# Performance work log

Hardware: AMD Instinct MI355X
Metric: run time of the kernel (lower is better)

Reference implementation:

```python
import jax, jax.numpy as jnp
import numpy as np

N, D, DFF, E, K = 2048, 1024, 4096, 8, 2  # tokens, d_model, d_ff, num_expert, top_k


def setup_inputs() -> dict:
    key = jax.random.key(0)
    ks = jax.random.split(key, 5)
    s = 0.02  # init scale
    return {
        "moe_inp": jax.random.normal(ks[0], (N, D), jnp.float32),
        "Wg": jax.random.normal(ks[1], (D, E), jnp.float32) * s,   # gate linear
        "bg": jnp.zeros((E,), jnp.float32),
        "W1": jax.random.normal(ks[2], (E, D, DFF), jnp.float32) * s,  # htoh4 per expert
        "b1": jnp.zeros((E, DFF), jnp.float32),
        "W2": jax.random.normal(ks[3], (E, DFF, D), jnp.float32) * s,  # h4toh per expert
        "b2": jnp.zeros((E, D), jnp.float32),
    }


def reference(moe_inp, Wg, bg, W1, b1, W2, b2):
    # --- NaiveGate: top-k experts per token, softmax over selected logits ---
    logits = moe_inp @ Wg + bg                      # [N, E]
    top_val, top_idx = jax.lax.top_k(logits, K)     # [N, K]
    score = jax.nn.softmax(top_val, axis=-1)        # [N, K]

    # Dense combine weights c[n, e] = sum_j score[n, j] * 1{top_idx[n, j] == e}.
    # This is the mathematically exact equivalent of scatter -> grouped expert
    # GEMM -> gather -> score-weighted combine in fmoe.
    comb = jnp.einsum(
        "nke,nk->ne", jax.nn.one_hot(top_idx, E, dtype=moe_inp.dtype), score
    )                                               # [N, E]

    # --- per-expert FFN: relu(x W1 + b1) W2 + b2, masked-combined by comb ---
    h = jax.nn.relu(jnp.einsum("nd,edh->enh", moe_inp, W1) + b1[:, None, :])  # [E, N, DFF]
    out = jnp.einsum("enh,ehd,ne->nd", h, W2, comb) + comb @ b2               # [N, D]
    return out
```

## Files before the change

### kernel.cpp

```cpp
#include <hip/hip_runtime.h>
#include <hip/hip_bf16.h>
#include <cstdint>
#include <cstddef>

#define NTOKS  2048
#define DMODEL 1024
#define DFFN   4096
#define NEXP   8
#define TSLOTS 40

typedef __attribute__((ext_vector_type(8))) short short8;
typedef __attribute__((ext_vector_type(4))) float f32x4;
typedef __attribute__((ext_vector_type(4))) unsigned short u16x4;
typedef __attribute__((ext_vector_type(8))) unsigned short u16x8;

static constexpr size_t alignup(size_t x) { return (x + 255) & ~(size_t)255; }
static constexpr size_t OFF_XB   = 0;
static constexpr size_t OFF_CNT  = alignup(OFF_XB + (size_t)(NTOKS + 1) * DMODEL * 2);
static constexpr size_t OFF_OFFS = OFF_CNT + 256;
static constexpr size_t OFF_TOKE = OFF_OFFS + 256;
static constexpr size_t OFF_TOKT = OFF_TOKE + (size_t)NTOKS * 2 * 4;
static constexpr size_t OFF_TOKS = OFF_TOKT + (size_t)NTOKS * 2 * 4;
static constexpr size_t OFF_TI   = alignup(OFF_TOKS + (size_t)NTOKS * 2 * 4);
static constexpr size_t OFF_CAP  = alignup(OFF_TI + 512);
static constexpr size_t OFF_H    = alignup(OFF_CAP + (size_t)NEXP * NTOKS * 4);
static constexpr size_t OFF_Y    = alignup(OFF_H + (size_t)(NTOKS * 2 + 128) * DFFN * 2);
static constexpr size_t OFF_WB   = alignup(OFF_Y + (size_t)2 * NTOKS * 2 * DMODEL * 4);

__device__ inline unsigned short f2bf(float f) {
  __hip_bfloat16 h = __float2bfloat16(f);
  return __builtin_bit_cast(unsigned short, h);
}

__device__ inline void gload16(const void* g, void* l) {
  __builtin_amdgcn_global_load_lds((const __attribute__((address_space(1))) unsigned int*)g,
                                   (__attribute__((address_space(3))) unsigned int*)l, 16, 0, 0);
}

__global__ __launch_bounds__(256) void k_convert(const float* __restrict__ x,
                                                 unsigned short* __restrict__ xb,
                                                 int* __restrict__ cnt) {
  if (blockIdx.x == 0 && threadIdx.x < NEXP) cnt[threadIdx.x] = 0;
  size_t base = ((size_t)blockIdx.x * 256 + threadIdx.x) * 8;
  const size_t total = (size_t)(NTOKS + 1) * DMODEL;
  if (base >= total) return;
  u16x8 o;
  if (base < (size_t)NTOKS * DMODEL) {
    f32x4 a = *(const f32x4*)(x + base);
    f32x4 b = *(const f32x4*)(x + base + 4);
#pragma unroll
    for (int j = 0; j < 4; ++j) { o[j] = f2bf(a[j]); o[4 + j] = f2bf(b[j]); }
  } else {
#pragma unroll
    for (int j = 0; j < 8; ++j) o[j] = 0;
  }
  *(u16x8*)(xb + base) = o;
}

template <int R, int C>
__global__ __launch_bounds__(256) void k_transconv(const float* __restrict__ W,
                                                   unsigned short* __restrict__ WT) {
  __shared__ unsigned short T[64][66];
  const int e = blockIdx.z;
  const int c0 = blockIdx.x * 64, r0 = blockIdx.y * 64;
  const float* Wp = W + (size_t)e * R * C;
  unsigned short* Tp = WT + (size_t)e * R * C;
  const int tid = threadIdx.x;
  const int rr = tid >> 4, cc = (tid & 15) << 2;
#pragma unroll
  for (int i = 0; i < 4; ++i) {
    int r = rr + (i << 4);
    f32x4 v = *(const f32x4*)(Wp + (size_t)(r0 + r) * C + c0 + cc);
    T[r][cc]     = f2bf(v[0]);
    T[r][cc + 1] = f2bf(v[1]);
    T[r][cc + 2] = f2bf(v[2]);
    T[r][cc + 3] = f2bf(v[3]);
  }
  __syncthreads();
  const int c = tid >> 2, kc = (tid & 3) << 4;
  u16x8 o0, o1;
#pragma unroll
  for (int i = 0; i < 8; ++i) { o0[i] = T[kc + i][c]; o1[i] = T[kc + 8 + i][c]; }
  unsigned short* dst = Tp + (size_t)(c0 + c) * R + r0 + kc;
  *(u16x8*)(dst) = o0;
  *(u16x8*)(dst + 8) = o1;
}

__global__ __launch_bounds__(256) void k_gate(const float* __restrict__ x,
                                              const float* __restrict__ Wg,
                                              const float* __restrict__ bg,
                                              int* __restrict__ cnt,
                                              int* __restrict__ tok_e,
                                              int* __restrict__ tok_t,
                                              float* __restrict__ tok_s,
                                              int* __restrict__ cap) {
  const int w = threadIdx.x >> 6, lane = threadIdx.x & 63;
  const int n = blockIdx.x * 4 + w;
  float acc[8];
#pragma unroll
  for (int e = 0; e < 8; ++e) acc[e] = 0.f;
  const float* xr = x + (size_t)n * DMODEL;
#pragma unroll 4
  for (int it = 0; it < DMODEL / 64; ++it) {
    int d = it * 64 + lane;
    float xv = xr[d];
    f32x4 w0 = *(const f32x4*)(Wg + d * 8);
    f32x4 w1 = *(const f32x4*)(Wg + d * 8 + 4);
#pragma unroll
    for (int j = 0; j < 4; ++j) { acc[j] += xv * w0[j]; acc[4 + j] += xv * w1[j]; }
  }
#pragma unroll
  for (int e = 0; e < 8; ++e)
#pragma unroll
    for (int off = 32; off; off >>= 1) acc[e] += __shfl_xor(acc[e], off, 64);
  if (lane == 0) {
    float l[8];
#pragma unroll
    for (int e = 0; e < 8; ++e) l[e] = acc[e] + bg[e];
    int i0 = 0; float v0 = l[0];
#pragma unroll
    for (int e = 1; e < 8; ++e) if (l[e] > v0) { v0 = l[e]; i0 = e; }
    int i1 = (i0 == 0) ? 1 : 0; float v1 = l[i1];
#pragma unroll
    for (int e = 0; e < 8; ++e) if (e != i0 && l[e] > v1) { v1 = l[e]; i1 = e; }
    float t = expf(v1 - v0);
    float inv = 1.f / (1.f + t);
    float s0 = inv, s1 = t * inv;
    int t0 = atomicAdd(&cnt[i0], 1);
    int t1 = atomicAdd(&cnt[i1], 1);
    cap[i0 * NTOKS + t0] = n;
    cap[i1 * NTOKS + t1] = n;
    tok_e[2 * n] = i0; tok_e[2 * n + 1] = i1;
    tok_t[2 * n] = t0; tok_t[2 * n + 1] = t1;
    tok_s[2 * n] = s0; tok_s[2 * n + 1] = s1;
  }
}

__global__ void k_scan(const int* __restrict__ cnt, int* __restrict__ offs,
                       int2* __restrict__ tinfo) {
  if (threadIdx.x == 0) {
    int s = 0;
#pragma unroll
    for (int e = 0; e < NEXP; ++e) { offs[e] = s; s += cnt[e]; }
    int ns = 0;
    for (int e = 0; e < NEXP; ++e)
      for (int t = 0; t * 128 < cnt[e]; ++t) { tinfo[ns] = make_int2(e, t * 128); ++ns; }
    for (; ns < TSLOTS; ++ns) tinfo[ns] = make_int2(-1, 0);
  }
}

template <int KTOT, int NTOT, int BN, bool FIRST, int KSPLIT>
__global__ __launch_bounds__(256) void k_gemm(const unsigned short* __restrict__ Asrc,
                                              const unsigned short* __restrict__ Bsrc,
                                              const float* __restrict__ bias,
                                              const int* __restrict__ cnt,
                                              const int* __restrict__ offs,
                                              const int2* __restrict__ tinfo,
                                              const int* __restrict__ cap,
                                              unsigned short* __restrict__ hout,
                                              float* __restrict__ yout) {
  const int2 ti = tinfo[blockIdx.y];
  if (ti.x < 0) return;
  const int e = ti.x, t0 = ti.y;
  const int c = cnt[e];
  const int base = offs[e] + t0;
  const int n0 = blockIdx.x * BN;
  constexpr int KCH = KTOT / KSPLIT;
  constexpr int NT = KCH / 32;
  const int kb = blockIdx.z * KCH;

  const int tid = threadIdx.x, w = tid >> 6, lane = tid & 63;
  const int l15 = lane & 15, lq = lane >> 4;
  constexpr int MR = 4;
  constexpr int NR = BN / 32;
  constexpr int BR = BN / 64;
  const int wr = w >> 1, wc = w & 1;

  __shared__ unsigned short As[2][128 * 32];
  __shared__ unsigned short Bs[2][BN * 32];

  const int rl = tid >> 2;
  const int sw = (((tid & 3) ^ (rl & 3) ^ ((rl >> 2) & 3)) << 3);
  const unsigned short* aptr[2];
#pragma unroll
  for (int r = 0; r < 2; ++r) {
    int row = r * 64 + rl;
    size_t gr;
    if constexpr (FIRST) gr = (size_t)((t0 + row < c) ? cap[e * NTOKS + t0 + row] : NTOKS);
    else                 gr = (size_t)(base + row);
    aptr[r] = Asrc + gr * (size_t)KTOT + kb + sw;
  }
  const unsigned short* Be = Bsrc + (size_t)e * ((size_t)KTOT * NTOT);
  const unsigned short* bptr[BR];
#pragma unroll
  for (int r = 0; r < BR; ++r)
    bptr[r] = Be + (size_t)(n0 + r * 64 + rl) * KTOT + kb + sw;

  auto stageA = [&](int k0, int b) {
#pragma unroll
    for (int r = 0; r < 2; ++r)
      gload16(aptr[r] + k0, &As[b][(r * 64 + w * 16) << 5]);
  };
  auto stageB = [&](int k0, int b) {
#pragma unroll
    for (int r = 0; r < BR; ++r)
      gload16(bptr[r] + k0, &Bs[b][(r * 64 + w * 16) << 5]);
  };

  f32x4 acc[MR][NR] = {};

  stageA(0, 0);
  stageB(0, 0);
  __syncthreads();

  int buf = 0;
  for (int t = 0; t < NT; ++t) {
    const int nxt = buf ^ 1;
    if (t + 1 < NT) { stageA((t + 1) * 32, nxt); stageB((t + 1) * 32, nxt); }

    short8 a[MR], b[NR];
    const int sw0 = ((lq ^ (l15 & 3) ^ ((l15 >> 2) & 3)) << 3);
#pragma unroll
    for (int m = 0; m < MR; ++m)
      a[m] = *(const short8*)&As[buf][((wr * 64 + m * 16 + l15) << 5) + sw0];
#pragma unroll
    for (int nn = 0; nn < NR; ++nn)
      b[nn] = *(const short8*)&Bs[buf][((wc * (BN / 2) + nn * 16 + l15) << 5) + sw0];
#pragma unroll
    for (int m = 0; m < MR; ++m)
#pragma unroll
      for (int nn = 0; nn < NR; ++nn)
        acc[m][nn] = __builtin_amdgcn_mfma_f32_16x16x32_bf16(a[m], b[nn], acc[m][nn], 0, 0, 0);

    __syncthreads();
    buf = nxt;
  }

  if constexpr (FIRST) {
    const float* be = bias + (size_t)e * NTOT;
#pragma unroll
    for (int m = 0; m < MR; ++m) {
#pragma unroll
      for (int q2 = 0; q2 < 4; ++q2) {
        int row = wr * 64 + m * 16 + lq * 4 + q2;
        if (t0 + row < c) {
          unsigned short* hr = hout + (size_t)(base + row) * NTOT;
#pragma unroll
          for (int nn = 0; nn < NR; ++nn) {
            int col = n0 + wc * (BN / 2) + nn * 16 + l15;
            float v = acc[m][nn][q2] + be[col];
            v = v > 0.f ? v : 0.f;
            hr[col] = f2bf(v);
          }
        }
      }
    }
  } else {
    float* yz = yout + (size_t)blockIdx.z * NTOKS * 2 * DMODEL;
#pragma unroll
    for (int m = 0; m < MR; ++m) {
#pragma unroll
      for (int q2 = 0; q2 < 4; ++q2) {
        int row = wr * 64 + m * 16 + lq * 4 + q2;
        if (t0 + row < c) {
          float* yr = yz + (size_t)(base + row) * NTOT;
#pragma unroll
          for (int nn = 0; nn < NR; ++nn) {
            int col = n0 + wc * (BN / 2) + nn * 16 + l15;
            yr[col] = acc[m][nn][q2];
          }
        }
      }
    }
  }
}

__global__ __launch_bounds__(256) void k_combine(const float* __restrict__ y,
                                                 const float* __restrict__ b2,
                                                 const int* __restrict__ tok_e,
                                                 const int* __restrict__ tok_t,
                                                 const float* __restrict__ tok_s,
                                                 const int* __restrict__ offs,
                                                 float* __restrict__ out) {
  const int n = blockIdx.x, t = threadIdx.x;
  const float* y1 = y + (size_t)NTOKS * 2 * DMODEL;
  const int e0 = tok_e[2 * n], e1 = tok_e[2 * n + 1];
  const int s0i = offs[e0] + tok_t[2 * n];
  const int s1i = offs[e1] + tok_t[2 * n + 1];
  const float sc0 = tok_s[2 * n], sc1 = tok_s[2 * n + 1];
  f32x4 v0 = *(const f32x4*)(y + (size_t)s0i * DMODEL + t * 4);
  f32x4 u0 = *(const f32x4*)(y1 + (size_t)s0i * DMODEL + t * 4);
  f32x4 v1 = *(const f32x4*)(y + (size_t)s1i * DMODEL + t * 4);
  f32x4 u1 = *(const f32x4*)(y1 + (size_t)s1i * DMODEL + t * 4);
  f32x4 c0 = *(const f32x4*)(b2 + (size_t)e0 * DMODEL + t * 4);
  f32x4 c1 = *(const f32x4*)(b2 + (size_t)e1 * DMODEL + t * 4);
  f32x4 r = sc0 * ((v0 + u0) + c0) + sc1 * ((v1 + u1) + c1);
  *(f32x4*)(out + (size_t)n * DMODEL + t * 4) = r;
}

extern "C" void kernel_launch(void* const* d_in, const int* in_sizes, int n_in,
                              void* d_out, int out_size, void* d_ws, size_t ws_size,
                              hipStream_t stream) {
  const float* x  = (const float*)d_in[0];
  const float* Wg = (const float*)d_in[1];
  const float* bg = (const float*)d_in[2];
  const float* W1 = (const float*)d_in[3];
  const float* b1 = (const float*)d_in[4];
  const float* W2 = (const float*)d_in[5];
  const float* b2 = (const float*)d_in[6];
  float* out = (float*)d_out;

  char* ws = (char*)d_ws;
  unsigned short* xb = (unsigned short*)(ws + OFF_XB);
  int*   cnt   = (int*)(ws + OFF_CNT);
  int*   offs  = (int*)(ws + OFF_OFFS);
  int*   tok_e = (int*)(ws + OFF_TOKE);
  int*   tok_t = (int*)(ws + OFF_TOKT);
  float* tok_s = (float*)(ws + OFF_TOKS);
  int2*  tinfo = (int2*)(ws + OFF_TI);
  int*   cap   = (int*)(ws + OFF_CAP);
  unsigned short* h  = (unsigned short*)(ws + OFF_H);
  float* y = (float*)(ws + OFF_Y);
  unsigned short* wb = (unsigned short*)(ws + OFF_WB);

  const int convBlocks = (int)(((size_t)(NTOKS + 1) * DMODEL / 8 + 255) / 256);
  k_convert<<<convBlocks, 256, 0, stream>>>(x, xb, cnt);
  k_gate<<<NTOKS / 4, 256, 0, stream>>>(x, Wg, bg, cnt, tok_e, tok_t, tok_s, cap);
  k_scan<<<1, 64, 0, stream>>>(cnt, offs, tinfo);

  k_transconv<DMODEL, DFFN><<<dim3(DFFN / 64, DMODEL / 64, NEXP), 256, 0, stream>>>(W1, wb);
  k_gemm<DMODEL, DFFN, 128, true, 1><<<dim3(DFFN / 128, TSLOTS, 1), 256, 0, stream>>>(
      xb, wb, b1, cnt, offs, tinfo, cap, h, nullptr);

  k_transconv<DFFN, DMODEL><<<dim3(DMODEL / 64, DFFN / 64, NEXP), 256, 0, stream>>>(W2, wb);
  k_gemm<DFFN, DMODEL, 64, false, 2><<<dim3(DMODEL / 64, TSLOTS, 2), 256, 0, stream>>>(
      h, wb, nullptr, cnt, offs, tinfo, cap, nullptr, y);

  k_combine<<<NTOKS, 256, 0, stream>>>(y, b2, tok_e, tok_t, tok_s, offs, out);
}
```

Before: 282.6 us.

## Merge prep kernels and overlap W2 conversion with first expert GEMM

Folds the W1 transpose/convert, input bf16 conversion and gating into one launch, and runs the first grouped GEMM and the W2 transpose/convert as one launch using separate weight buffers. This removes several launch boundaries and lets independent conversion work fill idle CUs during the GEMM. The counter reset moves to a memset. Y now aliases the W1 buffer, which is safe because W1 is dead by the time y is written. Mixed-role blocks share one grid, so LDS and register allocation follow the largest body, which may reduce occupancy.

```diff
diff --git a/kernel.cpp b/kernel.cpp
--- a/kernel.cpp
+++ b/kernel.cpp
@@ -7,7 +7,7 @@
 #define DMODEL 1024
 #define DFFN   4096
 #define NEXP   8
-#define TSLOTS 40
+#define TS128  40
 
 typedef __attribute__((ext_vector_type(8))) short short8;
 typedef __attribute__((ext_vector_type(4))) float f32x4;
@@ -21,11 +21,12 @@
 static constexpr size_t OFF_TOKE = OFF_OFFS + 256;
 static constexpr size_t OFF_TOKT = OFF_TOKE + (size_t)NTOKS * 2 * 4;
 static constexpr size_t OFF_TOKS = OFF_TOKT + (size_t)NTOKS * 2 * 4;
-static constexpr size_t OFF_TI   = alignup(OFF_TOKS + (size_t)NTOKS * 2 * 4);
-static constexpr size_t OFF_CAP  = alignup(OFF_TI + 512);
+static constexpr size_t OFF_TI2  = alignup(OFF_TOKS + (size_t)NTOKS * 2 * 4);
+static constexpr size_t OFF_CAP  = alignup(OFF_TI2 + TS128 * 8);
 static constexpr size_t OFF_H    = alignup(OFF_CAP + (size_t)NEXP * NTOKS * 4);
-static constexpr size_t OFF_Y    = alignup(OFF_H + (size_t)(NTOKS * 2 + 128) * DFFN * 2);
-static constexpr size_t OFF_WB   = alignup(OFF_Y + (size_t)2 * NTOKS * 2 * DMODEL * 4);
+static constexpr size_t OFF_WBA  = alignup(OFF_H + (size_t)(NTOKS * 2 + 128) * DFFN * 2);
+static constexpr size_t OFF_WBB  = alignup(OFF_WBA + (size_t)NEXP * DMODEL * DFFN * 2);
+static constexpr size_t OFF_Y    = OFF_WBA;
 
 __device__ inline unsigned short f2bf(float f) {
   __hip_bfloat16 h = __float2bfloat16(f);
@@ -37,11 +38,10 @@
                                    (__attribute__((address_space(3))) unsigned int*)l, 16, 0, 0);
 }
 
-__global__ __launch_bounds__(256) void k_convert(const float* __restrict__ x,
-                                                 unsigned short* __restrict__ xb,
-                                                 int* __restrict__ cnt) {
-  if (blockIdx.x == 0 && threadIdx.x < NEXP) cnt[threadIdx.x] = 0;
-  size_t base = ((size_t)blockIdx.x * 256 + threadIdx.x) * 8;
+
+__device__ __forceinline__ void conv_body(const float* __restrict__ x,
+                                          unsigned short* __restrict__ xb, int vb) {
+  size_t base = ((size_t)vb * 256 + threadIdx.x) * 8;
   const size_t total = (size_t)(NTOKS + 1) * DMODEL;
   if (base >= total) return;
   u16x8 o;
@@ -58,11 +58,12 @@
 }
 
 template <int R, int C>
-__global__ __launch_bounds__(256) void k_transconv(const float* __restrict__ W,
-                                                   unsigned short* __restrict__ WT) {
-  __shared__ unsigned short T[64][66];
-  const int e = blockIdx.z;
-  const int c0 = blockIdx.x * 64, r0 = blockIdx.y * 64;
+__device__ __forceinline__ void tc_body(const float* __restrict__ W,
+                                        unsigned short* __restrict__ WT,
+                                        int bx, int by, int bz,
+                                        unsigned short (*T)[66]) {
+  const int e = bz;
+  const int c0 = bx * 64, r0 = by * 64;
   const float* Wp = W + (size_t)e * R * C;
   unsigned short* Tp = WT + (size_t)e * R * C;
   const int tid = threadIdx.x;
@@ -86,16 +87,16 @@
   *(u16x8*)(dst + 8) = o1;
 }
 
-__global__ __launch_bounds__(256) void k_gate(const float* __restrict__ x,
-                                              const float* __restrict__ Wg,
-                                              const float* __restrict__ bg,
-                                              int* __restrict__ cnt,
-                                              int* __restrict__ tok_e,
-                                              int* __restrict__ tok_t,
-                                              float* __restrict__ tok_s,
-                                              int* __restrict__ cap) {
+__device__ __forceinline__ void gate_body(const float* __restrict__ x,
+                                          const float* __restrict__ Wg,
+                                          const float* __restrict__ bg,
+                                          int* __restrict__ cnt,
+                                          int* __restrict__ tok_e,
+                                          int* __restrict__ tok_t,
+                                          float* __restrict__ tok_s,
+                                          int* __restrict__ cap, int vb) {
   const int w = threadIdx.x >> 6, lane = threadIdx.x & 63;
-  const int n = blockIdx.x * 4 + w;
+  const int n = vb * 4 + w;
   float acc[8];
 #pragma unroll
   for (int e = 0; e < 8; ++e) acc[e] = 0.f;
@@ -136,16 +137,192 @@
   }
 }
 
+template <int KTOT, int NTOT, int BN, bool FIRST, int KSPLIT>
+__device__ __forceinline__ void gemm_body(const unsigned short* __restrict__ Asrc,
+                                          const unsigned short* __restrict__ Bsrc,
+                                          const float* __restrict__ bias,
+                                          const int* __restrict__ cnt,
+                                          const int* __restrict__ offs,
+                                          const int2* __restrict__ tinfo,
+                                          const int* __restrict__ cap,
+                                          unsigned short* __restrict__ hout,
+                                          float* __restrict__ yout,
+                                          int bx, int by, int bz, char* smem) {
+  const int2 ti = tinfo[by];
+  if (ti.x < 0) return;
+  const int e = ti.x, t0 = ti.y;
+  const int c = cnt[e];
+  const int base = offs[e] + t0;
+  const int n0 = bx * BN;
+  constexpr int KCH = KTOT / KSPLIT;
+  constexpr int NT = KCH / 32;
+  const int kb = bz * KCH;
+
+  const int tid = threadIdx.x, w = tid >> 6, lane = tid & 63;
+  const int l15 = lane & 15, lq = lane >> 4;
+  constexpr int MR = 4;
+  constexpr int NR = BN / 32;
+  constexpr int BR = BN / 64;
+  const int wr = w >> 1, wc = w & 1;
+
+  unsigned short (*As)[128 * 32] = (unsigned short (*)[128 * 32])smem;
+  unsigned short (*Bs)[BN * 32]  = (unsigned short (*)[BN * 32])(smem + 2 * 128 * 32 * 2);
+
+  const int rl = tid >> 2;
+  const int sw = (((tid & 3) ^ (rl & 3) ^ ((rl >> 2) & 3)) << 3);
+  const unsigned short* aptr[2];
+#pragma unroll
+  for (int r = 0; r < 2; ++r) {
+    int row = r * 64 + rl;
+    size_t gr;
+    if constexpr (FIRST) gr = (size_t)((t0 + row < c) ? cap[e * NTOKS + t0 + row] : NTOKS);
+    else                 gr = (size_t)(base + row);
+    aptr[r] = Asrc + gr * (size_t)KTOT + kb + sw;
+  }
+  const unsigned short* Be = Bsrc + (size_t)e * ((size_t)KTOT * NTOT);
+  const unsigned short* bptr[BR];
+#pragma unroll
+  for (int r = 0; r < BR; ++r)
+    bptr[r] = Be + (size_t)(n0 + r * 64 + rl) * KTOT + kb + sw;
+
+  auto stageA = [&](int k0, int b) {
+#pragma unroll
+    for (int r = 0; r < 2; ++r)
+      gload16(aptr[r] + k0, &As[b][(r * 64 + w * 16) << 5]);
+  };
+  auto stageB = [&](int k0, int b) {
+#pragma unroll
+    for (int r = 0; r < BR; ++r)
+      gload16(bptr[r] + k0, &Bs[b][(r * 64 + w * 16) << 5]);
+  };
+
+  f32x4 acc[MR][NR] = {};
+
+  stageA(0, 0);
+  stageB(0, 0);
+  __syncthreads();
+
+  int buf = 0;
+  for (int t = 0; t < NT; ++t) {
+    const int nxt = buf ^ 1;
+    if (t + 1 < NT) { stageA((t + 1) * 32, nxt); stageB((t + 1) * 32, nxt); }
+
+    short8 a[MR], b[NR];
+    const int sw0 = ((lq ^ (l15 & 3) ^ ((l15 >> 2) & 3)) << 3);
+#pragma unroll
+    for (int m = 0; m < MR; ++m)
+      a[m] = *(const short8*)&As[buf][((wr * 64 + m * 16 + l15) << 5) + sw0];
+#pragma unroll
+    for (int nn = 0; nn < NR; ++nn)
+      b[nn] = *(const short8*)&Bs[buf][((wc * (BN / 2) + nn * 16 + l15) << 5) + sw0];
+#pragma unroll
+    for (int m = 0; m < MR; ++m)
+#pragma unroll
+      for (int nn = 0; nn < NR; ++nn)
+        acc[m][nn] = __builtin_amdgcn_mfma_f32_16x16x32_bf16(a[m], b[nn], acc[m][nn], 0, 0, 0);
+
+    __syncthreads();
+    buf = nxt;
+  }
+
+  if constexpr (FIRST) {
+    const float* be = bias + (size_t)e * NTOT;
+#pragma unroll
+    for (int m = 0; m < MR; ++m) {
+#pragma unroll
+      for (int q2 = 0; q2 < 4; ++q2) {
+        int row = wr * 64 + m * 16 + lq * 4 + q2;
+        if (t0 + row < c) {
+          unsigned short* hr = hout + (size_t)(base + row) * NTOT;
+#pragma unroll
+          for (int nn = 0; nn < NR; ++nn) {
+            int col = n0 + wc * (BN / 2) + nn * 16 + l15;
+            float v = acc[m][nn][q2] + be[col];
+            v = v > 0.f ? v : 0.f;
+            hr[col] = f2bf(v);
+          }
+        }
+      }
+    }
+  } else {
+    float* yz = yout + (size_t)bz * NTOKS * 2 * DMODEL;
+#pragma unroll
+    for (int m = 0; m < MR; ++m) {
+#pragma unroll
+      for (int q2 = 0; q2 < 4; ++q2) {
+        int row = wr * 64 + m * 16 + lq * 4 + q2;
+        if (t0 + row < c) {
+          float* yr = yz + (size_t)(base + row) * NTOT;
+#pragma unroll
+          for (int nn = 0; nn < NR; ++nn) {
+            int col = n0 + wc * (BN / 2) + nn * 16 + l15;
+            yr[col] = acc[m][nn][q2];
+          }
+        }
+      }
+    }
+  }
+}
+
+
+__global__ __launch_bounds__(256) void k_phase1(const float* __restrict__ x,
+                                                const float* __restrict__ Wg,
+                                                const float* __restrict__ bg,
+                                                const float* __restrict__ W1,
+                                                unsigned short* __restrict__ xb,
+                                                unsigned short* __restrict__ wbA,
+                                                int* __restrict__ cnt,
+                                                int* __restrict__ tok_e,
+                                                int* __restrict__ tok_t,
+                                                float* __restrict__ tok_s,
+                                                int* __restrict__ cap) {
+  __shared__ unsigned short T[64][66];
+  constexpr int NTC1 = (DFFN / 64) * (DMODEL / 64) * NEXP;
+  constexpr int NCV  = (int)(((size_t)(NTOKS + 1) * DMODEL / 8 + 255) / 256);
+  const int b = blockIdx.x;
+  if (b < NTC1) {
+    const int bx = b & 63, by = (b >> 6) & 15, bz = b >> 10;
+    tc_body<DMODEL, DFFN>(W1, wbA, bx, by, bz, T);
+  } else if (b < NTC1 + NCV) {
+    conv_body(x, xb, b - NTC1);
+  } else {
+    gate_body(x, Wg, bg, cnt, tok_e, tok_t, tok_s, cap, b - NTC1 - NCV);
+  }
+}
+
 __global__ void k_scan(const int* __restrict__ cnt, int* __restrict__ offs,
-                       int2* __restrict__ tinfo) {
+                       int2* __restrict__ ti128) {
   if (threadIdx.x == 0) {
     int s = 0;
 #pragma unroll
     for (int e = 0; e < NEXP; ++e) { offs[e] = s; s += cnt[e]; }
-    int ns = 0;
+    int b = 0;
     for (int e = 0; e < NEXP; ++e)
-      for (int t = 0; t * 128 < cnt[e]; ++t) { tinfo[ns] = make_int2(e, t * 128); ++ns; }
-    for (; ns < TSLOTS; ++ns) tinfo[ns] = make_int2(-1, 0);
+      for (int t = 0; t * 128 < cnt[e]; ++t) { ti128[b] = make_int2(e, t * 128); ++b; }
+    for (; b < TS128; ++b) ti128[b] = make_int2(-1, 0);
+  }
+}
+
+__global__ __launch_bounds__(256) void k_phase3(const unsigned short* __restrict__ xb,
+                                                const unsigned short* __restrict__ wbA,
+                                                const float* __restrict__ b1,
+                                                const float* __restrict__ W2,
+                                                unsigned short* __restrict__ wbB,
+                                                const int* __restrict__ cnt,
+                                                const int* __restrict__ offs,
+                                                const int2* __restrict__ ti128,
+                                                const int* __restrict__ cap,
+                                                unsigned short* __restrict__ h) {
+  __shared__ __align__(16) char smem[2 * 128 * 32 * 2 + 2 * 128 * 32 * 2];
+  constexpr int NG1 = (DFFN / 128) * TS128;
+  const int b = blockIdx.x;
+  if (b < NG1) {
+    gemm_body<DMODEL, DFFN, 128, true, 1>(xb, wbA, b1, cnt, offs, ti128, cap, h, nullptr,
+                                          b & 31, b >> 5, 0, smem);
+  } else {
+    const int t = b - NG1;
+    const int bx = t & 15, by = (t >> 4) & 63, bz = t >> 10;
+    tc_body<DFFN, DMODEL>(W2, wbB, bx, by, bz, (unsigned short (*)[66])smem);
   }
 }
 
@@ -159,120 +336,9 @@
                                               const int* __restrict__ cap,
                                               unsigned short* __restrict__ hout,
                                               float* __restrict__ yout) {
-  const int2 ti = tinfo[blockIdx.y];
-  if (ti.x < 0) return;
-  const int e = ti.x, t0 = ti.y;
-  const int c = cnt[e];
-  const int base = offs[e] + t0;
-  const int n0 = blockIdx.x * BN;
-  constexpr int KCH = KTOT / KSPLIT;
-  constexpr int NT = KCH / 32;
-  const int kb = blockIdx.z * KCH;
-
-  const int tid = threadIdx.x, w = tid >> 6, lane = tid & 63;
-  const int l15 = lane & 15, lq = lane >> 4;
-  constexpr int MR = 4;
-  constexpr int NR = BN / 32;
-  constexpr int BR = BN / 64;
-  const int wr = w >> 1, wc = w & 1;
-
-  __shared__ unsigned short As[2][128 * 32];
-  __shared__ unsigned short Bs[2][BN * 32];
-
-  const int rl = tid >> 2;
-  const int sw = (((tid & 3) ^ (rl & 3) ^ ((rl >> 2) & 3)) << 3);
-  const unsigned short* aptr[2];
-#pragma unroll
-  for (int r = 0; r < 2; ++r) {
-    int row = r * 64 + rl;
-    size_t gr;
-    if constexpr (FIRST) gr = (size_t)((t0 + row < c) ? cap[e * NTOKS + t0 + row] : NTOKS);
-    else                 gr = (size_t)(base + row);
-    aptr[r] = Asrc + gr * (size_t)KTOT + kb + sw;
-  }
-  const unsigned short* Be = Bsrc + (size_t)e * ((size_t)KTOT * NTOT);
-  const unsigned short* bptr[BR];
-#pragma unroll
-  for (int r = 0; r < BR; ++r)
-    bptr[r] = Be + (size_t)(n0 + r * 64 + rl) * KTOT + kb + sw;
-
-  auto stageA = [&](int k0, int b) {
-#pragma unroll
-    for (int r = 0; r < 2; ++r)
-      gload16(aptr[r] + k0, &As[b][(r * 64 + w * 16) << 5]);
-  };
-  auto stageB = [&](int k0, int b) {
-#pragma unroll
-    for (int r = 0; r < BR; ++r)
-      gload16(bptr[r] + k0, &Bs[b][(r * 64 + w * 16) << 5]);
-  };
-
-  f32x4 acc[MR][NR] = {};
-
-  stageA(0, 0);
-  stageB(0, 0);
-  __syncthreads();
-
-  int buf = 0;
-  for (int t = 0; t < NT; ++t) {
-    const int nxt = buf ^ 1;
-    if (t + 1 < NT) { stageA((t + 1) * 32, nxt); stageB((t + 1) * 32, nxt); }
-
-    short8 a[MR], b[NR];
-    const int sw0 = ((lq ^ (l15 & 3) ^ ((l15 >> 2) & 3)) << 3);
-#pragma unroll
-    for (int m = 0; m < MR; ++m)
-      a[m] = *(const short8*)&As[buf][((wr * 64 + m * 16 + l15) << 5) + sw0];
-#pragma unroll
-    for (int nn = 0; nn < NR; ++nn)
-      b[nn] = *(const short8*)&Bs[buf][((wc * (BN / 2) + nn * 16 + l15) << 5) + sw0];
-#pragma unroll
-    for (int m = 0; m < MR; ++m)
-#pragma unroll
-      for (int nn = 0; nn < NR; ++nn)
-        acc[m][nn] = __builtin_amdgcn_mfma_f32_16x16x32_bf16(a[m], b[nn], acc[m][nn], 0, 0, 0);
-
-    __syncthreads();
-    buf = nxt;
-  }
-
-  if constexpr (FIRST) {
-    const float* be = bias + (size_t)e * NTOT;
-#pragma unroll
-    for (int m = 0; m < MR; ++m) {
-#pragma unroll
-      for (int q2 = 0; q2 < 4; ++q2) {
-        int row = wr * 64 + m * 16 + lq * 4 + q2;
-        if (t0 + row < c) {
-          unsigned short* hr = hout + (size_t)(base + row) * NTOT;
-#pragma unroll
-          for (int nn = 0; nn < NR; ++nn) {
-            int col = n0 + wc * (BN / 2) + nn * 16 + l15;
-            float v = acc[m][nn][q2] + be[col];
-            v = v > 0.f ? v : 0.f;
-            hr[col] = f2bf(v);
-          }
-        }
-      }
-    }
-  } else {
-    float* yz = yout + (size_t)blockIdx.z * NTOKS * 2 * DMODEL;
-#pragma unroll
-    for (int m = 0; m < MR; ++m) {
-#pragma unroll
-      for (int q2 = 0; q2 < 4; ++q2) {
-        int row = wr * 64 + m * 16 + lq * 4 + q2;
-        if (t0 + row < c) {
-          float* yr = yz + (size_t)(base + row) * NTOT;
-#pragma unroll
-          for (int nn = 0; nn < NR; ++nn) {
-            int col = n0 + wc * (BN / 2) + nn * 16 + l15;
-            yr[col] = acc[m][nn][q2];
-          }
-        }
-      }
-    }
-  }
+  __shared__ __align__(16) char smem[2 * 128 * 32 * 2 + 2 * BN * 32 * 2];
+  gemm_body<KTOT, NTOT, BN, FIRST, KSPLIT>(Asrc, Bsrc, bias, cnt, offs, tinfo, cap,
+                                           hout, yout, blockIdx.x, blockIdx.y, blockIdx.z, smem);
 }
 
 __global__ __launch_bounds__(256) void k_combine(const float* __restrict__ y,
@@ -317,24 +383,25 @@
   int*   tok_e = (int*)(ws + OFF_TOKE);
   int*   tok_t = (int*)(ws + OFF_TOKT);
   float* tok_s = (float*)(ws + OFF_TOKS);
-  int2*  tinfo = (int2*)(ws + OFF_TI);
+  int2*  ti128 = (int2*)(ws + OFF_TI2);
   int*   cap   = (int*)(ws + OFF_CAP);
-  unsigned short* h  = (unsigned short*)(ws + OFF_H);
+  unsigned short* h   = (unsigned short*)(ws + OFF_H);
+  unsigned short* wbA = (unsigned short*)(ws + OFF_WBA);
+  unsigned short* wbB = (unsigned short*)(ws + OFF_WBB);
   float* y = (float*)(ws + OFF_Y);
-  unsigned short* wb = (unsigned short*)(ws + OFF_WB);
-
-  const int convBlocks = (int)(((size_t)(NTOKS + 1) * DMODEL / 8 + 255) / 256);
-  k_convert<<<convBlocks, 256, 0, stream>>>(x, xb, cnt);
-  k_gate<<<NTOKS / 4, 256, 0, stream>>>(x, Wg, bg, cnt, tok_e, tok_t, tok_s, cap);
-  k_scan<<<1, 64, 0, stream>>>(cnt, offs, tinfo);
-
-  k_transconv<DMODEL, DFFN><<<dim3(DFFN / 64, DMODEL / 64, NEXP), 256, 0, stream>>>(W1, wb);
-  k_gemm<DMODEL, DFFN, 128, true, 1><<<dim3(DFFN / 128, TSLOTS, 1), 256, 0, stream>>>(
-      xb, wb, b1, cnt, offs, tinfo, cap, h, nullptr);
-
-  k_transconv<DFFN, DMODEL><<<dim3(DMODEL / 64, DFFN / 64, NEXP), 256, 0, stream>>>(W2, wb);
-  k_gemm<DFFN, DMODEL, 64, false, 2><<<dim3(DMODEL / 64, TSLOTS, 2), 256, 0, stream>>>(
-      h, wb, nullptr, cnt, offs, tinfo, cap, nullptr, y);
-
+
+  constexpr int NTC1 = (DFFN / 64) * (DMODEL / 64) * NEXP;
+  constexpr int NCV  = (int)(((size_t)(NTOKS + 1) * DMODEL / 8 + 255) / 256);
+  constexpr int NGT  = NTOKS / 4;
+  constexpr int NG1  = (DFFN / 128) * TS128;
+  constexpr int NTC2 = (DMODEL / 64) * (DFFN / 64) * NEXP;
+
+  hipMemsetAsync(ws + OFF_CNT, 0, 256, stream);
+  k_phase1<<<NTC1 + NCV + NGT, 256, 0, stream>>>(x, Wg, bg, W1, xb, wbA, cnt,
+                                                 tok_e, tok_t, tok_s, cap);
+  k_scan<<<1, 64, 0, stream>>>(cnt, offs, ti128);
+  k_phase3<<<NG1 + NTC2, 256, 0, stream>>>(xb, wbA, b1, W2, wbB, cnt, offs, ti128, cap, h);
+  k_gemm<DFFN, DMODEL, 64, false, 2><<<dim3(DMODEL / 64, TS128, 2), 256, 0, stream>>>(
+      h, wbB, nullptr, cnt, offs, ti128, cap, nullptr, y);
   k_combine<<<NTOKS, 256, 0, stream>>>(y, b2, tok_e, tok_t, tok_s, offs, out);
 }
```

Result: faster. 264.7 us (-6.3%).
